# Kernel optimization log

Hardware: AMD Instinct MI355X
Metric: run time of the kernel (lower is better)

## Reference

```python
import jax, jax.numpy as jnp
import numpy as np

N_HEADS = 16

def setup_inputs() -> dict:
    key = jax.random.key(0)
    ks = jax.random.split(key, 6)
    B, H, F, P, D = 2048, 1024, 4096, 512, 1024
    x = jax.random.normal(ks[0], (B, H), dtype=jnp.float32)
    # module inits features/prototypes ~ U(-0.27, 1)
    features = jax.random.uniform(ks[1], (F, D), minval=-0.27, maxval=1.0, dtype=jnp.float32)
    prototypes = jax.random.uniform(ks[2], (P, D), minval=-0.27, maxval=1.0, dtype=jnp.float32)
    # theta/alpha/beta are zero-init in the module; use small random values so output is non-trivial
    theta = jax.random.normal(ks[3], (N_HEADS, 1), dtype=jnp.float32)
    alpha = jax.random.normal(ks[4], (N_HEADS, 1), dtype=jnp.float32)
    beta = jax.random.normal(ks[5], (N_HEADS, 1), dtype=jnp.float32)
    return {"x": x, "features": features, "prototypes": prototypes,
            "theta": theta, "alpha": alpha, "beta": beta}

def reference(x, features, prototypes, theta, alpha, beta):
    n_heads = N_HEADS
    B, total_dim = x.shape
    d = total_dim // n_heads
    xh = x.reshape(B, n_heads, d)                       # b h d
    fh = features.reshape(-1, n_heads, d).transpose(1, 0, 2)    # h f d
    ph = prototypes.reshape(-1, n_heads, d).transpose(1, 0, 2)  # h p d
    x_features = jnp.einsum('bhd,hfd->bhf', xh, fh)     # [B,h,F]
    p_features = jnp.einsum('hpd,hfd->hpf', ph, fh)     # [h,P,F]
    x_present = jax.nn.relu(x_features)
    p_present = jax.nn.relu(p_features)
    x_weighted = x_features * x_present
    p_weighted = p_features * p_present
    # head-batched GEMMs sharing operands
    common = jnp.einsum('bhf,hpf->bhp', x_weighted, p_weighted)
    x_p_interaction = jnp.einsum('bhf,hpf->bhp', x_weighted, p_present)
    p_x_interaction = jnp.einsum('bhf,hpf->bhp', x_present, p_weighted)
    x_weighted_sum = x_weighted.sum(axis=2, keepdims=True)      # [B,h,1]
    p_weighted_sum = p_weighted.sum(axis=2)[None, :, :]         # [1,h,P]
    x_distinctive = x_weighted_sum - x_p_interaction
    p_distinctive = p_weighted_sum - p_x_interaction
    th = theta.reshape(1, n_heads, 1)
    al = alpha.reshape(1, n_heads, 1)
    be = beta.reshape(1, n_heads, 1)
    out = th * common - al * x_distinctive - be * p_distinctive  # [B,h,P]
    return out.reshape(B, -1)
```

## Files before the change

### kernel.cpp

```cpp
#include <hip/hip_runtime.h>
#include <cstdint>

#define NH 16
#define DH 64
#define FF 4096
#define PP 512
#define BB 2048

typedef __bf16 bf16x8 __attribute__((ext_vector_type(8)));
typedef float f32x4 __attribute__((ext_vector_type(4)));
typedef float fl4 __attribute__((ext_vector_type(4)));
typedef unsigned short us4 __attribute__((ext_vector_type(4)));
typedef unsigned int u32x2 __attribute__((ext_vector_type(2)));

__device__ __forceinline__ unsigned short f2bf(float f) {
  unsigned u = __float_as_uint(f);
  u += 0x7FFFu + ((u >> 16) & 1u);
  return (unsigned short)(u >> 16);
}

__device__ __forceinline__ unsigned int pkbf(float lo, float hi) {
  unsigned a = __float_as_uint(lo) + 0x8000u;
  unsigned b = __float_as_uint(hi) + 0x8000u;
  return __builtin_amdgcn_perm(b, a, 0x07060302u);
}

__device__ __forceinline__ void gload_lds16(const void* g, void* l) {
  __builtin_amdgcn_global_load_lds(
      (const __attribute__((address_space(1))) void*)g,
      (__attribute__((address_space(3))) void*)(unsigned int)(unsigned long long)l,
      16, 0, 0);
}

__global__ void cvt_fp(const float* __restrict__ f, const float* __restrict__ p,
                       unsigned short* __restrict__ fb,
                       unsigned short* __restrict__ pb) {
  const int nf = FF * 1024 / 4, np = PP * 1024 / 4;
  int i = blockIdx.x * blockDim.x + threadIdx.x;
  const fl4* src;
  us4* dst;
  if (i < nf) {
    src = (const fl4*)f + i;
    dst = (us4*)fb + i;
  } else if (i < nf + np) {
    src = (const fl4*)p + (i - nf);
    dst = (us4*)pb + (i - nf);
  } else {
    return;
  }
  fl4 v = *src;
  us4 o;
  o.x = f2bf(v.x); o.y = f2bf(v.y); o.z = f2bf(v.z); o.w = f2bf(v.w);
  *dst = o;
}

__global__ __launch_bounds__(256, 2) void gemm_proto(
    const unsigned short* __restrict__ Abf, const unsigned short* __restrict__ Fbf,
    unsigned short* __restrict__ O1, unsigned short* __restrict__ O2,
    float* __restrict__ pws,
    const float* __restrict__ theta, const float* __restrict__ alpha,
    const float* __restrict__ beta) {
  const int h = blockIdx.z;
  const int n0 = blockIdx.x * 128;
  const int lm0 = blockIdx.y * 128;
  const int t = threadIdx.x;

  __shared__ __align__(16) char As[128 * 128];
  __shared__ __align__(16) char Bs[128 * 128];

  {
    const char* ab = (const char*)(Abf + (size_t)lm0 * 1024 + h * 64);
    const char* bb = (const char*)(Fbf + (size_t)n0 * 1024 + h * 64);
#pragma unroll
    for (int r = 0; r < 4; ++r) {
      int o = r * 4096 + t * 16;
      int row = o >> 7, col = o & 127;
      gload_lds16(ab + (size_t)row * 2048 + col, As + o);
      gload_lds16(bb + (size_t)row * 2048 + col, Bs + o);
    }
  }
  __syncthreads();

  const int wave = t >> 6, lane = t & 63;
  const int wm = wave & 1, wn = wave >> 1;
  const int quad = lane >> 4, lr = lane & 15;

  f32x4 acc[4][4];
#pragma unroll
  for (int i = 0; i < 4; ++i)
#pragma unroll
    for (int j = 0; j < 4; ++j) acc[i][j] = (f32x4){0.f, 0.f, 0.f, 0.f};

#pragma unroll
  for (int s = 0; s < 2; ++s) {
    bf16x8 av[4], bv[4];
#pragma unroll
    for (int fm = 0; fm < 4; ++fm) {
      int row = wm * 64 + fm * 16 + lr;
      av[fm] = *(const bf16x8*)(As + row * 128 + s * 64 + quad * 16);
    }
#pragma unroll
    for (int fn = 0; fn < 4; ++fn) {
      int row = wn * 64 + fn * 16 + lr;
      bv[fn] = *(const bf16x8*)(Bs + row * 128 + s * 64 + quad * 16);
    }
#pragma unroll
    for (int fm = 0; fm < 4; ++fm)
#pragma unroll
      for (int fn = 0; fn < 4; ++fn)
        acc[fm][fn] = __builtin_amdgcn_mfma_f32_16x16x32_bf16(av[fm], bv[fn],
                                                              acc[fm][fn], 0, 0, 0);
  }

  const float th = theta[h], al = alpha[h], be = beta[h];

#pragma unroll
  for (int fm = 0; fm < 4; ++fm) {
    int prow = lm0 + wm * 64 + fm * 16 + quad * 4;
    float rs0 = 0.f, rs1 = 0.f, rs2 = 0.f, rs3 = 0.f;
#pragma unroll
    for (int fn = 0; fn < 4; ++fn) {
      int f = n0 + wn * 64 + fn * 16 + lr;
#pragma unroll
      for (int i = 0; i < 4; ++i) {
        float pf = acc[fm][fn][i];
        float pp = fmaxf(pf, 0.f);
        float pw = pf * pp;
        size_t idx = ((size_t)(h * PP + prow + i)) * FF + f;
        O1[idx] = f2bf(th * pw + al * pp - al);
        O2[idx] = f2bf(be * pw);
        if (i == 0) rs0 += pw;
        else if (i == 1) rs1 += pw;
        else if (i == 2) rs2 += pw;
        else rs3 += pw;
      }
    }
    float rs[4] = {rs0, rs1, rs2, rs3};
#pragma unroll
    for (int i = 0; i < 4; ++i) {
      float s = rs[i];
      s += __shfl_xor(s, 1);
      s += __shfl_xor(s, 2);
      s += __shfl_xor(s, 4);
      s += __shfl_xor(s, 8);
      if (lr == 0) atomicAdd(&pws[h * PP + prow + i], be * s);
    }
  }
}

__global__ __launch_bounds__(256, 2) void fused_main(
    const float* __restrict__ x, const unsigned short* __restrict__ f_bf,
    const unsigned short* __restrict__ Q1, const unsigned short* __restrict__ Q2,
    const float* __restrict__ pws, float* __restrict__ out) {
  const int l = blockIdx.x;
  const int i = l >> 3;
  const int g = (l & 7) * 4 + (i & 3);
  const int h = g >> 1;
  const int n0 = (g & 1) * 256;
  const int m0 = (i >> 2) * 128;
  const int t = threadIdx.x;
  const int wave = t >> 6, lane = t & 63;
  const int quad = lane >> 4, lr = lane & 15;
  const int key8 = lr & 7;
  const int key2 = (lr >> 1) & 3;

  __shared__ __align__(16) char sF[2 * 4096];
  __shared__ __align__(16) char sXw[2 * 8192];
  __shared__ __align__(16) char sXp[2 * 8192];

  bf16x8 xh[2][2];
#pragma unroll
  for (int bn = 0; bn < 2; ++bn)
#pragma unroll
    for (int s = 0; s < 2; ++s) {
      int b = m0 + wave * 32 + bn * 16 + lr;
      const float* xr = x + (size_t)b * 1024 + h * 64 + s * 32 + quad * 8;
      fl4 v0 = *(const fl4*)xr;
      fl4 v1 = *(const fl4*)(xr + 4);
      union { unsigned u[4]; bf16x8 v; } cv;
      cv.u[0] = pkbf(v0.x, v0.y);
      cv.u[1] = pkbf(v0.z, v0.w);
      cv.u[2] = pkbf(v1.x, v1.y);
      cv.u[3] = pkbf(v1.z, v1.w);
      xh[bn][s] = cv.v;
    }

  int af_off[2][2];
#pragma unroll
  for (int fm = 0; fm < 2; ++fm)
#pragma unroll
    for (int s = 0; s < 2; ++s)
      af_off[fm][s] = (fm * 16 + lr) * 128 + (((s * 4 + quad) ^ key8) * 16);

  int cw_off[2][2];
#pragma unroll
  for (int fm = 0; fm < 2; ++fm)
#pragma unroll
    for (int bn = 0; bn < 2; ++bn)
      cw_off[fm][bn] = (wave * 32 + bn * 16 + lr) * 64 +
                       (((fm * 2 + (quad >> 1)) ^ key2) * 16) + (quad & 1) * 8;

  int aw_off[8];
#pragma unroll
  for (int fm = 0; fm < 8; ++fm)
    aw_off[fm] = (fm * 16 + lr) * 64 + ((quad ^ key2) * 16);

  const char* srcF;
  {
    int row = t >> 3, c = t & 7, cs = c ^ (row & 7);
    srcF = (const char*)f_bf + h * 128 + (size_t)row * 2048 + cs * 16;
  }

  const char* qb1 = (const char*)Q1 + (size_t)(h * PP + n0) * FF * 2;
  const char* qb2 = (const char*)Q2 + (size_t)(h * PP + n0) * FF * 2;
  unsigned qo = (unsigned)(((wave * 64 + lr) * FF + quad * 8) * 2);

  f32x4 acc[8][4];
#pragma unroll
  for (int i2 = 0; i2 < 8; ++i2)
#pragma unroll
    for (int j = 0; j < 4; ++j) acc[i2][j] = (f32x4){0.f, 0.f, 0.f, 0.f};

  f32x4 xf[2][2];

#define BSTEP(SFB) do {                                                      \
    _Pragma("unroll") for (int fm_ = 0; fm_ < 2; ++fm_)                      \
      _Pragma("unroll") for (int bn_ = 0; bn_ < 2; ++bn_)                    \
        xf[fm_][bn_] = (f32x4){0.f, 0.f, 0.f, 0.f};                          \
    _Pragma("unroll") for (int s_ = 0; s_ < 2; ++s_)                         \
      _Pragma("unroll") for (int fm_ = 0; fm_ < 2; ++fm_) {                  \
        bf16x8 af_ = *(const bf16x8*)(sF + (SFB) + af_off[fm_][s_]);         \
        _Pragma("unroll") for (int bn_ = 0; bn_ < 2; ++bn_)                  \
          xf[fm_][bn_] = __builtin_amdgcn_mfma_f32_16x16x32_bf16(            \
              af_, xh[bn_][s_], xf[fm_][bn_], 0, 0, 0);                      \
      }                                                                      \
  } while (0)

#define CPACK(FM, BN, XB) do {                                               \
    float v0_ = xf[FM][BN][0], v1_ = xf[FM][BN][1];                          \
    float v2_ = xf[FM][BN][2], v3_ = xf[FM][BN][3];                          \
    float p0_ = fmaxf(v0_, 0.f), p1_ = fmaxf(v1_, 0.f);                      \
    float p2_ = fmaxf(v2_, 0.f), p3_ = fmaxf(v3_, 0.f);                      \
    u32x2 w_, p_;                                                            \
    w_.x = pkbf(v0_ * p0_, v1_ * p1_);                                       \
    w_.y = pkbf(v2_ * p2_, v3_ * p3_);                                       \
    p_.x = pkbf(p0_, p1_);                                                   \
    p_.y = pkbf(p2_, p3_);                                                   \
    *(u32x2*)(sXw + (XB) + cw_off[FM][BN]) = w_;                             \
    *(u32x2*)(sXp + (XB) + cw_off[FM][BN]) = p_;                             \
  } while (0)

#define DREAD(HF, XA) do {                                                   \
    _Pragma("unroll") for (int fm_ = 0; fm_ < 4; ++fm_) {                    \
      aw[fm_] = *(const bf16x8*)(sXw + (XA) + aw_off[(HF) * 4 + fm_]);       \
      ap[fm_] = *(const bf16x8*)(sXp + (XA) + aw_off[(HF) * 4 + fm_]);       \
    }                                                                        \
  } while (0)

#define DMFMA(HF, FNP) do {                                                  \
    _Pragma("unroll") for (int f2_ = 0; f2_ < 2; ++f2_) {                    \
      const int fn_ = (FNP) * 2 + f2_;                                       \
      _Pragma("unroll") for (int fm_ = 0; fm_ < 4; ++fm_) {                  \
        acc[(HF) * 4 + fm_][fn_] = __builtin_amdgcn_mfma_f32_16x16x32_bf16(  \
            aw[fm_], q1v[fn_], acc[(HF) * 4 + fm_][fn_], 0, 0, 0);           \
        acc[(HF) * 4 + fm_][fn_] = __builtin_amdgcn_mfma_f32_16x16x32_bf16(  \
            ap[fm_], q2v[fn_], acc[(HF) * 4 + fm_][fn_], 0, 0, 0);           \
      }                                                                      \
    }                                                                        \
  } while (0)

  gload_lds16(srcF, sF + t * 16);
  srcF += 32 * 2048;
  asm volatile("s_waitcnt vmcnt(0)\n\ts_barrier" ::: "memory");
  __builtin_amdgcn_sched_barrier(0);
  gload_lds16(srcF, sF + 4096 + t * 16);
  srcF += 32 * 2048;
  BSTEP(0);
  CPACK(0, 0, 0);
  CPACK(0, 1, 0);
  CPACK(1, 0, 0);
  CPACK(1, 1, 0);
  asm volatile("s_waitcnt vmcnt(0) lgkmcnt(0)\n\ts_barrier" ::: "memory");
  __builtin_amdgcn_sched_barrier(0);

  for (int it = 0; it < FF / 32; ++it) {
    const int pA = it & 1;
    const int pB = pA ^ 1;
    const int xa = pA * 8192, xb = pB * 8192;

    bf16x8 q1v[4], q2v[4];
#pragma unroll
    for (int fn = 0; fn < 4; ++fn) {
      q1v[fn] = *(const bf16x8*)(qb1 + qo + fn * 131072);
      q2v[fn] = *(const bf16x8*)(qb2 + qo + fn * 131072);
    }
    qo += 64;

    gload_lds16(srcF, sF + pA * 4096 + t * 16);
    srcF += 32 * 2048;

    BSTEP(pB * 4096);
    bf16x8 aw[4], ap[4];
    DREAD(0, xa);
    __builtin_amdgcn_sched_barrier(0);

    __builtin_amdgcn_s_setprio(1);
    CPACK(0, 0, xb);
    DMFMA(0, 0);
    __builtin_amdgcn_sched_barrier(0);
    CPACK(0, 1, xb);
    DMFMA(0, 1);
    DREAD(1, xa);
    __builtin_amdgcn_sched_barrier(0);
    CPACK(1, 0, xb);
    DMFMA(1, 0);
    __builtin_amdgcn_sched_barrier(0);
    CPACK(1, 1, xb);
    DMFMA(1, 1);
    __builtin_amdgcn_s_setprio(0);

    asm volatile("s_waitcnt vmcnt(0) lgkmcnt(0)\n\ts_barrier" ::: "memory");
    __builtin_amdgcn_sched_barrier(0);
  }

#pragma unroll
  for (int fn = 0; fn < 4; ++fn) {
    int p = n0 + wave * 64 + fn * 16 + lr;
    float sub = pws[h * PP + p];
#pragma unroll
    for (int fm = 0; fm < 8; ++fm) {
      int brow = m0 + fm * 16 + quad * 4;
#pragma unroll
      for (int i2 = 0; i2 < 4; ++i2) {
        out[(size_t)(brow + i2) * (NH * PP) + h * PP + p] = acc[fm][fn][i2] - sub;
      }
    }
  }
}

extern "C" void kernel_launch(void* const* d_in, const int* in_sizes, int n_in,
                              void* d_out, int out_size, void* d_ws, size_t ws_size,
                              hipStream_t stream) {
  const float* x = (const float*)d_in[0];
  const float* features = (const float*)d_in[1];
  const float* prototypes = (const float*)d_in[2];
  const float* theta = (const float*)d_in[3];
  const float* alpha = (const float*)d_in[4];
  const float* beta = (const float*)d_in[5];
  float* out = (float*)d_out;

  char* ws = (char*)d_ws;
  size_t off = 0;
  auto carve = [&](size_t bytes) -> char* {
    char* p = ws + off;
    off += (bytes + 255) & ~(size_t)255;
    return p;
  };
  unsigned short* f_bf = (unsigned short*)carve((size_t)(FF + 64) * 1024 * 2);
  unsigned short* p_bf = (unsigned short*)carve((size_t)PP * 1024 * 2);
  unsigned short* Q1 = (unsigned short*)carve((size_t)NH * PP * FF * 2);
  unsigned short* Q2 = (unsigned short*)carve((size_t)NH * PP * FF * 2);
  float* pws = (float*)carve((size_t)NH * PP * 4);

  const int ncvt = (FF + PP) * 1024 / 4;
  cvt_fp<<<(ncvt + 255) / 256, 256, 0, stream>>>(features, prototypes, f_bf, p_bf);
  hipMemsetAsync(pws, 0, (size_t)NH * PP * 4, stream);

  gemm_proto<<<dim3(FF / 128, PP / 128, NH), 256, 0, stream>>>(
      p_bf, f_bf, Q1, Q2, pws, theta, alpha, beta);

  fused_main<<<dim3(512, 1, 1), 256, 0, stream>>>(
      x, f_bf, Q1, Q2, pws, out);
}
```

Measured before the change: 383.0 us.

## Switch main GEMM to 32x32x16 MFMA and prefetch Q operands one iteration ahead

Replaces the 16x16x32 bf16 MFMA tiles in the main accumulation with 32x32x16 MFMA tiles, which changes the accumulator layout, the LDS read offsets and the output write mapping. The global loads of Q1/Q2 move to the end of each iteration, so the next step's operands are fetched while the barrier wait runs with vmcnt(8) instead of vmcnt(0). The loop is unrolled by two so the double-buffer indices become compile-time constants. The aim is fewer MFMA issues and fewer LDS reads per FLOP, plus hiding global-load latency, at the cost of register pressure and a fragile vmcnt count.

```diff
diff --git a/kernel.cpp b/kernel.cpp
--- a/kernel.cpp
+++ b/kernel.cpp
@@ -9,6 +9,7 @@
 
 typedef __bf16 bf16x8 __attribute__((ext_vector_type(8)));
 typedef float f32x4 __attribute__((ext_vector_type(4)));
+typedef float f32x16 __attribute__((ext_vector_type(16)));
 typedef float fl4 __attribute__((ext_vector_type(4)));
 typedef unsigned short us4 __attribute__((ext_vector_type(4)));
 typedef unsigned int u32x2 __attribute__((ext_vector_type(2)));
@@ -161,6 +162,7 @@
   const int t = threadIdx.x;
   const int wave = t >> 6, lane = t & 63;
   const int quad = lane >> 4, lr = lane & 15;
+  const int el = lane & 31, half = lane >> 5;
   const int key8 = lr & 7;
   const int key2 = (lr >> 1) & 3;
 
@@ -200,10 +202,13 @@
       cw_off[fm][bn] = (wave * 32 + bn * 16 + lr) * 64 +
                        (((fm * 2 + (quad >> 1)) ^ key2) * 16) + (quad & 1) * 8;
 
-  int aw_off[8];
-#pragma unroll
-  for (int fm = 0; fm < 8; ++fm)
-    aw_off[fm] = (fm * 16 + lr) * 64 + ((quad ^ key2) * 16);
+  int axk[2];
+  {
+    int keyel = ((el & 15) >> 1) & 3;
+#pragma unroll
+    for (int ks = 0; ks < 2; ++ks)
+      axk[ks] = el * 64 + (((ks * 2 + half) ^ keyel) * 16);
+  }
 
   const char* srcF;
   {
@@ -213,15 +218,19 @@
 
   const char* qb1 = (const char*)Q1 + (size_t)(h * PP + n0) * FF * 2;
   const char* qb2 = (const char*)Q2 + (size_t)(h * PP + n0) * FF * 2;
-  unsigned qo = (unsigned)(((wave * 64 + lr) * FF + quad * 8) * 2);
-
-  f32x4 acc[8][4];
-#pragma unroll
-  for (int i2 = 0; i2 < 8; ++i2)
-#pragma unroll
-    for (int j = 0; j < 4; ++j) acc[i2][j] = (f32x4){0.f, 0.f, 0.f, 0.f};
+  unsigned qo = (unsigned)(((wave * 64 + el) * FF + half * 8) * 2);
+
+  f32x16 acc[4][2];
+#pragma unroll
+  for (int mt = 0; mt < 4; ++mt)
+#pragma unroll
+    for (int nt = 0; nt < 2; ++nt)
+#pragma unroll
+      for (int r = 0; r < 16; ++r) acc[mt][nt][r] = 0.f;
 
   f32x4 xf[2][2];
+  bf16x8 q1v[2][2], q2v[2][2];
+  bf16x8 awf[2][2], apf[2][2];
 
 #define BSTEP(SFB) do {                                                      \
     _Pragma("unroll") for (int fm_ = 0; fm_ < 2; ++fm_)                      \
@@ -250,23 +259,63 @@
     *(u32x2*)(sXp + (XB) + cw_off[FM][BN]) = p_;                             \
   } while (0)
 
-#define DREAD(HF, XA) do {                                                   \
-    _Pragma("unroll") for (int fm_ = 0; fm_ < 4; ++fm_) {                    \
-      aw[fm_] = *(const bf16x8*)(sXw + (XA) + aw_off[(HF) * 4 + fm_]);       \
-      ap[fm_] = *(const bf16x8*)(sXp + (XA) + aw_off[(HF) * 4 + fm_]);       \
-    }                                                                        \
-  } while (0)
-
-#define DMFMA(HF, FNP) do {                                                  \
-    _Pragma("unroll") for (int f2_ = 0; f2_ < 2; ++f2_) {                    \
-      const int fn_ = (FNP) * 2 + f2_;                                       \
-      _Pragma("unroll") for (int fm_ = 0; fm_ < 4; ++fm_) {                  \
-        acc[(HF) * 4 + fm_][fn_] = __builtin_amdgcn_mfma_f32_16x16x32_bf16(  \
-            aw[fm_], q1v[fn_], acc[(HF) * 4 + fm_][fn_], 0, 0, 0);           \
-        acc[(HF) * 4 + fm_][fn_] = __builtin_amdgcn_mfma_f32_16x16x32_bf16(  \
-            ap[fm_], q2v[fn_], acc[(HF) * 4 + fm_][fn_], 0, 0, 0);           \
+#define DREAD32(P, XA) do {                                                  \
+    _Pragma("unroll") for (int m_ = 0; m_ < 2; ++m_)                         \
+      _Pragma("unroll") for (int ks_ = 0; ks_ < 2; ++ks_) {                  \
+        awf[m_][ks_] =                                                       \
+            *(const bf16x8*)(sXw + (XA) + (P) * 4096 + m_ * 2048 + axk[ks_]);\
+        apf[m_][ks_] =                                                       \
+            *(const bf16x8*)(sXp + (XA) + (P) * 4096 + m_ * 2048 + axk[ks_]);\
       }                                                                      \
-    }                                                                        \
+  } while (0)
+
+#define DM32(P, KS) do {                                                     \
+    _Pragma("unroll") for (int m_ = 0; m_ < 2; ++m_)                         \
+      _Pragma("unroll") for (int nt_ = 0; nt_ < 2; ++nt_) {                  \
+        acc[(P) * 2 + m_][nt_] = __builtin_amdgcn_mfma_f32_32x32x16_bf16(    \
+            awf[m_][KS], q1v[nt_][KS], acc[(P) * 2 + m_][nt_], 0, 0, 0);     \
+        acc[(P) * 2 + m_][nt_] = __builtin_amdgcn_mfma_f32_32x32x16_bf16(    \
+            apf[m_][KS], q2v[nt_][KS], acc[(P) * 2 + m_][nt_], 0, 0, 0);     \
+      }                                                                      \
+  } while (0)
+
+#define QLOAD() do {                                                         \
+    _Pragma("unroll") for (int nt_ = 0; nt_ < 2; ++nt_)                      \
+      _Pragma("unroll") for (int ks_ = 0; ks_ < 2; ++ks_) {                  \
+        q1v[nt_][ks_] =                                                      \
+            *(const bf16x8*)(qb1 + qo + nt_ * 262144 + ks_ * 32);            \
+        q2v[nt_][ks_] =                                                      \
+            *(const bf16x8*)(qb2 + qo + nt_ * 262144 + ks_ * 32);            \
+      }                                                                      \
+  } while (0)
+
+#define BODY(PA_, PB_) do {                                                  \
+    gload_lds16(srcF, sF + (PA_) * 4096 + t * 16);                           \
+    srcF += 32 * 2048;                                                       \
+    BSTEP((PB_) * 4096);                                                     \
+    DREAD32(0, (PA_) * 8192);                                                \
+    __builtin_amdgcn_sched_barrier(0);                                       \
+    __builtin_amdgcn_s_setprio(1);                                           \
+    CPACK(0, 0, (PB_) * 8192);                                               \
+    DM32(0, 0);                                                              \
+    __builtin_amdgcn_sched_barrier(0);                                       \
+    CPACK(0, 1, (PB_) * 8192);                                               \
+    DM32(0, 1);                                                              \
+    DREAD32(1, (PA_) * 8192);                                                \
+    __builtin_amdgcn_sched_barrier(0);                                       \
+    CPACK(1, 0, (PB_) * 8192);                                               \
+    DM32(1, 0);                                                              \
+    __builtin_amdgcn_sched_barrier(0);                                       \
+    CPACK(1, 1, (PB_) * 8192);                                               \
+    DM32(1, 1);                                                              \
+    __builtin_amdgcn_s_setprio(0);                                           \
+    QLOAD();                                                                 \
+    qo += 64;                                                                \
+      \
+      \
+      \
+    asm volatile("s_waitcnt vmcnt(8) lgkmcnt(0)\n\ts_barrier" ::: "memory"); \
+    __builtin_amdgcn_sched_barrier(0);                                       \
   } while (0)
 
   gload_lds16(srcF, sF + t * 16);
@@ -280,59 +329,29 @@
   CPACK(0, 1, 0);
   CPACK(1, 0, 0);
   CPACK(1, 1, 0);
-  asm volatile("s_waitcnt vmcnt(0) lgkmcnt(0)\n\ts_barrier" ::: "memory");
+  QLOAD();
+  qo += 64;
+  asm volatile("s_waitcnt vmcnt(8) lgkmcnt(0)\n\ts_barrier" ::: "memory");
   __builtin_amdgcn_sched_barrier(0);
 
-  for (int it = 0; it < FF / 32; ++it) {
-    const int pA = it & 1;
-    const int pB = pA ^ 1;
-    const int xa = pA * 8192, xb = pB * 8192;
-
-    bf16x8 q1v[4], q2v[4];
-#pragma unroll
-    for (int fn = 0; fn < 4; ++fn) {
-      q1v[fn] = *(const bf16x8*)(qb1 + qo + fn * 131072);
-      q2v[fn] = *(const bf16x8*)(qb2 + qo + fn * 131072);
-    }
-    qo += 64;
-
-    gload_lds16(srcF, sF + pA * 4096 + t * 16);
-    srcF += 32 * 2048;
-
-    BSTEP(pB * 4096);
-    bf16x8 aw[4], ap[4];
-    DREAD(0, xa);
-    __builtin_amdgcn_sched_barrier(0);
-
-    __builtin_amdgcn_s_setprio(1);
-    CPACK(0, 0, xb);
-    DMFMA(0, 0);
-    __builtin_amdgcn_sched_barrier(0);
-    CPACK(0, 1, xb);
-    DMFMA(0, 1);
-    DREAD(1, xa);
-    __builtin_amdgcn_sched_barrier(0);
-    CPACK(1, 0, xb);
-    DMFMA(1, 0);
-    __builtin_amdgcn_sched_barrier(0);
-    CPACK(1, 1, xb);
-    DMFMA(1, 1);
-    __builtin_amdgcn_s_setprio(0);
-
-    asm volatile("s_waitcnt vmcnt(0) lgkmcnt(0)\n\ts_barrier" ::: "memory");
-    __builtin_amdgcn_sched_barrier(0);
-  }
-
-#pragma unroll
-  for (int fn = 0; fn < 4; ++fn) {
-    int p = n0 + wave * 64 + fn * 16 + lr;
+  for (int it2 = 0; it2 < FF / 64; ++it2) {
+    BODY(0, 1);
+    BODY(1, 0);
+  }
+
+#pragma unroll
+  for (int nt = 0; nt < 2; ++nt) {
+    int p = n0 + wave * 64 + nt * 32 + el;
     float sub = pws[h * PP + p];
 #pragma unroll
-    for (int fm = 0; fm < 8; ++fm) {
-      int brow = m0 + fm * 16 + quad * 4;
-#pragma unroll
-      for (int i2 = 0; i2 < 4; ++i2) {
-        out[(size_t)(brow + i2) * (NH * PP) + h * PP + p] = acc[fm][fn][i2] - sub;
+    for (int mt = 0; mt < 4; ++mt) {
+#pragma unroll
+      for (int gi = 0; gi < 4; ++gi) {
+#pragma unroll
+        for (int r = 0; r < 4; ++r) {
+          int b = m0 + mt * 32 + gi * 8 + half * 4 + r;
+          out[(size_t)b * (NH * PP) + h * PP + p] = acc[mt][nt][gi * 4 + r] - sub;
+        }
       }
     }
   }
```

Measured after the change: 395.9 us. 3.4% more time.
